# Optimization experiments

Measured on AMD Instinct MI355X. Metric: run time of the kernel, lower is better.

## Reference

```python
import jax, jax.numpy as jnp
import numpy as np

B, S = 32, 256


def _lsa(cost):
    """Rectangular linear sum assignment (Jonker-Volgenant shortest augmenting path),
    equivalent to scipy.optimize.linear_sum_assignment. cost: [R, C] numpy."""
    cost = np.asarray(cost, dtype=np.float64)
    transposed = cost.shape[0] > cost.shape[1]
    if transposed:
        cost = cost.T
    nr, nc = cost.shape  # nr <= nc
    u = np.zeros(nr)
    v = np.zeros(nc)
    path = np.full(nc, -1, dtype=np.int64)
    col4row = np.full(nr, -1, dtype=np.int64)
    row4col = np.full(nc, -1, dtype=np.int64)
    for cur_row in range(nr):
        min_val = 0.0
        i = cur_row
        remaining = np.arange(nc)
        sp = np.full(nc, np.inf)
        SR = np.zeros(nr, dtype=bool)
        SC = np.zeros(nc, dtype=bool)
        sink = -1
        while sink == -1:
            SR[i] = True
            r = min_val + cost[i, remaining] - u[i] - v[remaining]
            better = r < sp[remaining]
            idx_b = remaining[better]
            sp[idx_b] = r[better]
            path[idx_b] = i
            k = int(np.argmin(sp[remaining]))
            j = int(remaining[k])
            min_val = float(sp[j])
            if row4col[j] == -1:
                sink = j
            else:
                i = int(row4col[j])
                SC[j] = True
                remaining = np.delete(remaining, k)
        u[cur_row] += min_val
        others = SR.copy()
        others[cur_row] = False
        rr = np.where(others)[0]
        u[rr] += min_val - sp[col4row[rr]]
        cc = np.where(SC)[0]
        v[cc] += sp[cc] - min_val
        j = sink
        while True:
            i = int(path[j])
            row4col[j] = i
            col4row[i], j = j, int(col4row[i])
            if i == cur_row:
                break
    if transposed:
        rows = col4row
        cols = np.arange(nr)
        order = np.argsort(rows)
        return rows[order], cols[order]
    return np.arange(nr), col4row


def _match(cost_np, valid_np):
    """Per-sample Hungarian matching restricted to valid GT columns.
    Returns padded (pred_idx, gt_idx) [B, maxG] and ngt [B]."""
    Bn = cost_np.shape[0]
    ngt = valid_np.sum(axis=1).astype(np.int64)
    maxG = max(int(ngt.max()), 1)
    pi = np.zeros((Bn, maxG), dtype=np.int64)
    gi = np.zeros((Bn, maxG), dtype=np.int64)
    for b in range(Bn):
        cols = np.where(valid_np[b])[0]
        if len(cols) == 0:
            continue
        r, c = _lsa(cost_np[b][:, cols])
        pi[b, : len(r)] = r
        gi[b, : len(c)] = cols[c]
    return pi, gi, ngt


def _bce_clipped(p, t):
    # matches torch BCELoss: log terms clamped at -100
    return -(t * jnp.clip(jnp.log(p), -100.0) + (1.0 - t) * jnp.clip(jnp.log(1.0 - p), -100.0))


def _loss(pred_strokes, pred_validity, targets, pi, gi, ngt):
    gt_strokes = targets[..., :10]
    gt_val = targets[..., 10:11]
    Bn, maxG = pi.shape
    ngt_f = jnp.asarray(ngt, dtype=pred_strokes.dtype)
    mask = (jnp.arange(maxG)[None, :] < jnp.asarray(ngt)[:, None]).astype(pred_strokes.dtype)  # [B, maxG]
    bidx = np.arange(Bn)[:, None]
    mp = pred_strokes[bidx, pi]  # [B, maxG, 10]
    mg = gt_strokes[bidx, gi]    # [B, maxG, 10]
    # per-sample L1 means over matched pairs (coord: first 8 dims, width: last 2)
    coord = (jnp.abs(mp[..., :8] - mg[..., :8]).sum(-1) * mask).sum(-1) / jnp.maximum(ngt_f * 8.0, 1.0)
    width = (jnp.abs(mp[..., 8:10] - mg[..., 8:10]).sum(-1) * mask).sum(-1) / jnp.maximum(ngt_f * 2.0, 1.0)
    bce = _bce_clipped(pred_validity, gt_val).mean(axis=(1, 2))  # global validity BCE per sample
    # if num_gt == 0 the original only adds the validity BCE
    loss_b = jnp.where(ngt_f > 0, 5.0 * coord + 1.0 * width + 1.0 * bce, bce)
    return loss_b.mean()


def setup_inputs() -> dict:
    key = jax.random.key(0)
    k1, k2, k3, k4 = jax.random.split(key, 4)
    pred_strokes = jax.random.normal(k1, (B, S, 10), dtype=jnp.float32)
    pred_validity = jax.random.uniform(k2, (B, S, 1), dtype=jnp.float32, minval=1e-4, maxval=1.0 - 1e-4)
    gt_strokes = jax.random.normal(k3, (B, S, 10), dtype=jnp.float32)
    gt_valid = (jax.random.uniform(k4, (B, S, 1)) < 0.3).astype(jnp.float32)
    targets = jnp.concatenate([gt_strokes, gt_valid], axis=-1)
    return {"pred_strokes": pred_strokes, "pred_validity": pred_validity, "targets": targets}


def reference(pred_strokes, pred_validity, targets):
    gt_strokes = targets[..., :10]
    gt_val = targets[..., 10:11]
    # vectorized pairwise cost: 5 * L1(coord) + 1 * L1(width), [B, S, S]
    coord_c = jnp.abs(pred_strokes[:, :, None, :8] - gt_strokes[:, None, :, :8]).sum(-1)
    width_c = jnp.abs(pred_strokes[:, :, None, 8:10] - gt_strokes[:, None, :, 8:10]).sum(-1)
    cost = 5.0 * coord_c + width_c
    pi, gi, ngt = _match(np.asarray(cost), np.asarray(gt_val[..., 0]) > 0.5)
    return _loss(pred_strokes, pred_validity, targets, pi, gi, ngt)
```

## Files before the change

### kernel.cpp

```cpp
#include <hip/hip_runtime.h>
#include <math.h>

#define BN 32
#define SN 256
#define CAP 96
#define NT  256

#define KINF 0xFF800000u
#define KMAX 0xFFFFFFFFu

__device__ __forceinline__ unsigned f2k(float f) {
    unsigned b = __float_as_uint(f);
    return (b & 0x80000000u) ? ~b : (b | 0x80000000u);
}
__device__ __forceinline__ float k2f(unsigned k) {
    unsigned b = (k & 0x80000000u) ? (k ^ 0x80000000u) : ~k;
    return __uint_as_float(b);
}
__device__ __forceinline__ int sel4(int a0, int a1, int a2, int a3, int s) {
    int x01 = (s & 1) ? a1 : a0;
    int x23 = (s & 1) ? a3 : a2;
    return (s & 2) ? x23 : x01;
}
#define DPP_MIN(x, ctrl) do {                                                    \
    unsigned _t = (unsigned)__builtin_amdgcn_update_dpp((int)(x), (int)(x),      \
                                                        (ctrl), 0xF, 0xF, false);\
    if (_t < (x)) (x) = _t;                                                      \
} while (0)
#define DPP_MIN2(m1, m2, ctrl) do {                                              \
    unsigned _o1 = (unsigned)__builtin_amdgcn_update_dpp(-1, (int)(m1),          \
                                                         (ctrl), 0xF, 0xF, false);\
    unsigned _o2 = (unsigned)__builtin_amdgcn_update_dpp(-1, (int)(m2),          \
                                                         (ctrl), 0xF, 0xF, false);\
    unsigned _hi = (m1) > _o1 ? (m1) : _o1;                                      \
    (m1) = (m1) < _o1 ? (m1) : _o1;                                              \
    unsigned _s  = (m2) < _o2 ? (m2) : _o2;                                      \
    (m2) = _s < _hi ? _s : _hi;                                                  \
} while (0)
#define DPP_CHAIN_MIN2(a,b) do { DPP_MIN2(a,b,0x111); DPP_MIN2(a,b,0x112); DPP_MIN2(a,b,0x114); \
                                 DPP_MIN2(a,b,0x118); DPP_MIN2(a,b,0x142); DPP_MIN2(a,b,0x143); } while (0)

__device__ __forceinline__ unsigned waveMinU32(unsigned x) {
    DPP_MIN(x, 0x111); DPP_MIN(x, 0x112); DPP_MIN(x, 0x114); DPP_MIN(x, 0x118);
    unsigned a = (unsigned)__builtin_amdgcn_readlane((int)x, 15);
    unsigned b = (unsigned)__builtin_amdgcn_readlane((int)x, 31);
    unsigned c = (unsigned)__builtin_amdgcn_readlane((int)x, 47);
    unsigned d = (unsigned)__builtin_amdgcn_readlane((int)x, 63);
    unsigned ab = a < b ? a : b, cd = c < d ? c : d;
    return ab < cd ? ab : cd;
}

__device__ __forceinline__ float costf(const float* pb, const float* gc) {
    float c = 0.f;
    #pragma unroll
    for (int d = 0; d < 8; ++d) c += fabsf(pb[d] - gc[d]);
    float w = fabsf(pb[8] - gc[8]) + fabsf(pb[9] - gc[9]);
    return 5.0f * c + w;
}
__device__ __forceinline__ void pickLowest(unsigned long long n0, unsigned long long n1,
                                           unsigned long long n2, unsigned long long n3,
                                           int& lm, int& slot) {
    int l0 = n0 ? __builtin_ctzll(n0) : 64;
    int l1 = n1 ? __builtin_ctzll(n1) : 64;
    int l2 = n2 ? __builtin_ctzll(n2) : 64;
    int l3 = n3 ? __builtin_ctzll(n3) : 64;
    int a  = l0 < l1 ? l0 : l1;
    int c  = l2 < l3 ? l2 : l3;
    lm   = a < c ? a : c;
    slot = (l0 == lm) ? 0 : (l1 == lm) ? 1 : (l2 == lm) ? 2 : 3;
}

__global__ __launch_bounds__(NT) void detr_kernel(
    const float* __restrict__ pred_strokes,
    const float* __restrict__ pred_validity,
    const float* __restrict__ targets,
    float* __restrict__ out)
{
    extern __shared__ __align__(16) float sC[];
    __shared__ __align__(16) float sPred[SN * 10];
    __shared__ __align__(16) float sRowC[SN * 10];
    __shared__ float sU[SN];
    __shared__ float sVal[SN];
    __shared__ int   sJ[SN];
    __shared__ int   sFree[SN];
    __shared__ int   sCr4[SN];
    __shared__ float sRed[12];
    __shared__ int   sNgt;

    const int b = blockIdx.x, tid = threadIdx.x, lane = tid & 63, wid = tid >> 6;

    {
        const float4* gp = (const float4*)(pred_strokes + (size_t)b * SN * 10);
        float4* sp4 = (float4*)sPred;
        for (int t = tid; t < SN * 10 / 4; t += NT) sp4[t] = gp[t];
        const float4* gt = (const float4*)(targets + (size_t)b * SN * 11);
        float4* st4 = (float4*)sC;
        for (int t = tid; t < SN * 11 / 4; t += NT) st4[t] = gt[t];
    }
    __syncthreads();

    if (wid == 0) {
        const float* tmpT = sC;
        int ng = 0;
        #pragma unroll
        for (int s = 0; s < 4; ++s) {
            int   pos = s * 64 + lane;
            float tv  = tmpT[pos * 11 + 10];
            sVal[pos] = tv;
            bool  val = tv > 0.5f;
            unsigned long long m = __ballot(val);
            if (val) {
                int r = ng + (int)__popcll(m & ((1ull << lane) - 1ull));
                #pragma unroll
                for (int d = 0; d < 10; ++d) sRowC[r * 10 + d] = tmpT[pos * 11 + d];
            }
            ng += (int)__popcll(m);
        }
        if (lane == 0) sNgt = ng;
    }
    __syncthreads();
    const int ngt = sNgt;

    __align__(16) float prf[40];
    #pragma unroll
    for (int t = 0; t < 10; ++t) ((float4*)prf)[t] = ((const float4*)sPred)[lane * 10 + t];

    float bces;
    {
        float pv  = pred_validity[(size_t)b * SN + tid];
        float tv  = sVal[tid];
        float lp  = logf(pv);       if (lp  < -100.f) lp  = -100.f;
        float l1p = logf(1.f - pv); if (l1p < -100.f) l1p = -100.f;
        bces = -(tv * lp + (1.f - tv) * l1p);
    }

    for (int r = wid; r < ngt; r += 4) {
        const float* gp = &sRowC[r * 10];
        float gc[10];
        #pragma unroll
        for (int d = 0; d < 10; ++d) gc[d] = gp[d];
        float4 cc;
        cc.x = costf(prf +  0, gc);
        cc.y = costf(prf + 10, gc);
        cc.z = costf(prf + 20, gc);
        cc.w = costf(prf + 30, gc);
        if (r < CAP) ((float4*)sC)[r * 64 + lane] = cc;

        unsigned q0 = f2k(cc.x), q1 = f2k(cc.y), q2 = f2k(cc.z), q3 = f2k(cc.w);
        unsigned bk = q0; int bs = 0;
        if (q1 < bk) { bk = q1; bs = 1; }
        if (q2 < bk) { bk = q2; bs = 2; }
        if (q3 < bk) { bk = q3; bs = 3; }
        unsigned minK = waveMinU32(bk);
        unsigned long long mm = __ballot(bk == minK);
        int lm   = __builtin_ctzll(mm);
        int slot = __builtin_amdgcn_readlane(bs, lm);
        if (lane == 0) { sU[r] = k2f(minK); sJ[r] = lm * 4 + slot; }
    }
    __syncthreads();

    if (wid == 0) {
        float v0 = 0.f, v1 = 0.f, v2 = 0.f, v3 = 0.f;
        int   rv0 = -1, rv1 = -1, rv2 = -1, rv3 = -1;
        int   cr0 = -1, cr1 = -1, cr2 = -1, cr3 = -1;
        int   p0 = -1, p1 = -1, p2 = -1, p3 = -1;
        float sc0 = 0.f, sc1 = 0.f, sc2 = 0.f, sc3 = 0.f;
        int   nfree = 0;

        #define ASSIGN_COL(J, R) { int _l=(J)>>2, _s=(J)&3; bool _o=(lane==_l);      \
            switch(_s){ case 0: if(_o) rv0=(R); break; case 1: if(_o) rv1=(R); break;\
                        case 2: if(_o) rv2=(R); break; default: if(_o) rv3=(R); } }
        #define ASSIGN_ROW(R, J) { int _l=(R)>>2, _s=(R)&3; bool _o=(lane==_l);      \
            switch(_s){ case 0: if(_o) cr0=(J); break; case 1: if(_o) cr1=(J); break;\
                        case 2: if(_o) cr2=(J); break; default: if(_o) cr3=(J); } }
        #define READ_RV(LM, SL) __builtin_amdgcn_readlane(sel4(rv0,rv1,rv2,rv3,(SL)), (LM))
        #define LOADROW(I, CW)                                                   \
            if ((I) < CAP) (CW) = ((const float4*)sC)[(I) * 64 + lane];          \
            else {                                                               \
                float gc[10];                                                    \
                _Pragma("unroll")                                                \
                for (int d = 0; d < 10; ++d) gc[d] = sRowC[(I) * 10 + d];        \
                (CW).x = costf(prf +  0, gc); (CW).y = costf(prf + 10, gc);      \
                (CW).z = costf(prf + 20, gc); (CW).w = costf(prf + 30, gc);      \
            }

        int jr[4];
        #pragma unroll
        for (int s = 0; s < 4; ++s) jr[s] = sJ[s * 64 + lane];

        for (int r = 0; r < ngt; ++r) {
            int js = __builtin_amdgcn_readlane(sel4(jr[0], jr[1], jr[2], jr[3], r >> 6), r & 63);
            int lm = js >> 2, slot = js & 3;
            int rn = READ_RV(lm, slot);
            if (rn < 0) {
                ASSIGN_COL(js, r)
                ASSIGN_ROW(r, js)
            } else {
                if (lane == 0) sFree[nfree] = r;
                nfree++;
            }
        }

        int cnt = nfree;
        for (int pass = 0; pass < 2 && cnt > 0; ++pass) {
            int newc = 0;
            for (int idx = 0; idx < cnt; ++idx) {
                const int r = sFree[idx];
                float4 cw;
                LOADROW(r, cw)
                unsigned q0 = f2k(cw.x - v0), q1 = f2k(cw.y - v1);
                unsigned q2 = f2k(cw.z - v2), q3 = f2k(cw.w - v3);
                unsigned a1 = q0 < q1 ? q0 : q1, a2 = q0 < q1 ? q1 : q0;
                unsigned b1 = q2 < q3 ? q2 : q3, b2 = q2 < q3 ? q3 : q2;
                unsigned m1 = a1 < b1 ? a1 : b1;
                unsigned hi = a1 < b1 ? b1 : a1;
                unsigned l2 = a2 < b2 ? a2 : b2;
                unsigned m2 = l2 < hi ? l2 : hi;
                DPP_CHAIN_MIN2(m1, m2);
                unsigned u1k = (unsigned)__builtin_amdgcn_readlane((int)m1, 63);
                unsigned u2k = (unsigned)__builtin_amdgcn_readlane((int)m2, 63);

                unsigned long long n0 = __ballot(q0 == u1k);
                unsigned long long n1 = __ballot(q1 == u1k);
                unsigned long long n2 = __ballot(q2 == u1k);
                unsigned long long n3 = __ballot(q3 == u1k);
                int lm, slot;
                pickLowest(n0, n1, n2, n3, lm, slot);
                int j1 = lm * 4 + slot;
                int i1 = READ_RV(lm, slot);

                if (u1k != u2k) {
                    float du = k2f(u1k) - k2f(u2k);
                    bool own = (lane == (j1 >> 2));
                    switch (j1 & 3) {
                        case 0:  if (own) v0 += du; break;
                        case 1:  if (own) v1 += du; break;
                        case 2:  if (own) v2 += du; break;
                        default: if (own) v3 += du; break;
                    }
                    if (lane == 0) sU[r] = k2f(u2k);
                } else {
                    if (i1 >= 0) {
                        switch (slot) {
                            case 0:  n0 &= ~(1ull << lm); break;
                            case 1:  n1 &= ~(1ull << lm); break;
                            case 2:  n2 &= ~(1ull << lm); break;
                            default: n3 &= ~(1ull << lm); break;
                        }
                        pickLowest(n0, n1, n2, n3, lm, slot);
                        j1 = lm * 4 + slot;
                        i1 = READ_RV(lm, slot);
                    }
                    if (lane == 0) sU[r] = k2f(u1k);
                }

                ASSIGN_COL(j1, r)
                ASSIGN_ROW(r, j1)
                if (i1 >= 0) {
                    if (lane == 0) sFree[newc] = i1;
                    newc++;
                }
            }
            cnt = newc;
        }

        for (int fi = 0; fi < cnt; ++fi) {
            const int cur = sFree[fi];
            unsigned k0 = KINF, k1 = KINF, k2 = KINF, k3 = KINF;
            int   scm  = 0;
            float minv = 0.f;
            int   i    = cur;
            int   sink;

            float4 cw;
            LOADROW(i, cw)
            float ui = sU[i];

            for (;;) {
                #define RELAX(S, CS, KS, PS, VS)                                 \
                {                                                                \
                    float rr = ((minv + CS) - ui) - VS;                          \
                    unsigned kr = f2k(rr);                                       \
                    bool upd = (kr < KS) && !((scm >> S) & 1);                   \
                    if (upd) { KS = kr; PS = i; }                                \
                }
                RELAX(0, cw.x, k0, p0, v0)
                RELAX(1, cw.y, k1, p1, v1)
                RELAX(2, cw.z, k2, p2, v2)
                RELAX(3, cw.w, k3, p3, v3)
                #undef RELAX

                unsigned bk = k0 < k1 ? k0 : k1;
                unsigned bc = k2 < k3 ? k2 : k3;
                if (bc < bk) bk = bc;
                unsigned minK = waveMinU32(bk);

                unsigned long long m0 = __ballot(k0 == minK);
                unsigned long long m1m = __ballot(k1 == minK);
                unsigned long long m2m = __ballot(k2 == minK);
                unsigned long long m3m = __ballot(k3 == minK);
                int lm, slot;
                pickLowest(m0, m1m, m2m, m3m, lm, slot);
                int bj = lm * 4 + slot;

                int rn = READ_RV(lm, slot);
                if (rn < 0) { sink = bj; minv = k2f(minK); break; }
                i = rn;

                float4 cw2;
                LOADROW(i, cw2)
                float ui2 = sU[i];

                minv = k2f(minK);
                bool own = (lane == lm);
                switch (slot) {
                    case 0:  if (own) { scm |= 1; k0 = KMAX; sc0 = minv; } break;
                    case 1:  if (own) { scm |= 2; k1 = KMAX; sc1 = minv; } break;
                    case 2:  if (own) { scm |= 4; k2 = KMAX; sc2 = minv; } break;
                    default: if (own) { scm |= 8; k3 = KMAX; sc3 = minv; } break;
                }
                cw = cw2; ui = ui2;
            }

            if (lane == 0) sU[cur] += minv;
            if (scm & 1) { sU[rv0] += minv - sc0; v0 += sc0 - minv; }
            if (scm & 2) { sU[rv1] += minv - sc1; v1 += sc1 - minv; }
            if (scm & 4) { sU[rv2] += minv - sc2; v2 += sc2 - minv; }
            if (scm & 8) { sU[rv3] += minv - sc3; v3 += sc3 - minv; }

            int j = sink;
            for (;;) {
                int sj = j & 3, lj = j >> 2;
                int i2 = __builtin_amdgcn_readlane(sel4(p0, p1, p2, p3, sj), lj);
                ASSIGN_COL(j, i2)
                int si = i2 & 3, li = i2 >> 2;
                int tmp = __builtin_amdgcn_readlane(sel4(cr0, cr1, cr2, cr3, si), li);
                ASSIGN_ROW(i2, j)
                j = tmp;
                if (i2 == cur) break;
            }
        }

        ((int4*)sCr4)[lane] = make_int4(cr0, cr1, cr2, cr3);
    }
    __syncthreads();

    float coordv = 0.f, widthv = 0.f;
    if (tid < ngt) {
        int p = sCr4[tid];
        const float* pp = &sPred[p * 10];
        const float* gg = &sRowC[tid * 10];
        float c = 0.f;
        #pragma unroll
        for (int d = 0; d < 8; ++d) c += fabsf(pp[d] - gg[d]);
        coordv = c;
        widthv = fabsf(pp[8] - gg[8]) + fabsf(pp[9] - gg[9]);
    }
    #pragma unroll
    for (int m = 1; m <= 32; m <<= 1) {
        coordv += __shfl_xor(coordv, m, 64);
        widthv += __shfl_xor(widthv, m, 64);
        bces   += __shfl_xor(bces,   m, 64);
    }
    if (lane == 0) {
        sRed[wid * 3 + 0] = coordv;
        sRed[wid * 3 + 1] = widthv;
        sRed[wid * 3 + 2] = bces;
    }
    __syncthreads();
    if (tid == 0) {
        float C = 0.f, W = 0.f, Bc = 0.f;
        #pragma unroll
        for (int w = 0; w < 4; ++w) {
            C += sRed[w * 3 + 0]; W += sRed[w * 3 + 1]; Bc += sRed[w * 3 + 2];
        }
        float bcem = Bc / (float)SN;
        float lb = (ngt > 0)
                 ? (5.f * C / (8.f * (float)ngt) + W / (2.f * (float)ngt) + bcem)
                 : bcem;
        atomicAdd(out, lb * (1.0f / (float)BN));
    }
}

extern "C" void kernel_launch(void* const* d_in, const int* in_sizes, int n_in,
                              void* d_out, int out_size, void* d_ws, size_t ws_size,
                              hipStream_t stream) {
    const float* pred_strokes  = (const float*)d_in[0];
    const float* pred_validity = (const float*)d_in[1];
    const float* targets       = (const float*)d_in[2];
    float* out = (float*)d_out;

    const int dynBytes = CAP * SN * 4;
    (void)hipFuncSetAttribute((const void*)detr_kernel,
                              hipFuncAttributeMaxDynamicSharedMemorySize, dynBytes);
    detr_kernel<<<BN, NT, dynBytes, stream>>>(pred_strokes, pred_validity, targets, out);
}
```

Measured before the change: 123.4 us.

## Use packed value-index wave argmin and parallel atomic column claiming in init

Replaces the separate wave min reduction and four-ballot argmin with a single DPP reduction over (key, column) pairs, which returns the minimum and its lowest column index together inside the Dijkstra loop. The serial column-reduction pass that assigned each row's best column one by one is replaced by per-wave atomicMin claims into shared memory, followed by a ballot-compacted free-row list built in parallel. This shortens the serial critical path of the single-wave assignment. The pair reduction costs two DPP moves per step plus 64-bit compares, and the claiming order (lowest row wins) differs from the previous sequential first-come rule.

New measurement: 115.0 us. 1.07x faster.

```diff
diff --git a/kernel.cpp b/kernel.cpp
--- a/kernel.cpp
+++ b/kernel.cpp
@@ -8,6 +8,7 @@
 
 #define KINF 0xFF800000u
 #define KMAX 0xFFFFFFFFu
+#define CLNONE 0x7FFFFFFF
 
 __device__ __forceinline__ unsigned f2k(float f) {
     unsigned b = __float_as_uint(f);
@@ -40,14 +41,31 @@
 #define DPP_CHAIN_MIN2(a,b) do { DPP_MIN2(a,b,0x111); DPP_MIN2(a,b,0x112); DPP_MIN2(a,b,0x114); \
                                  DPP_MIN2(a,b,0x118); DPP_MIN2(a,b,0x142); DPP_MIN2(a,b,0x143); } while (0)
 
-__device__ __forceinline__ unsigned waveMinU32(unsigned x) {
-    DPP_MIN(x, 0x111); DPP_MIN(x, 0x112); DPP_MIN(x, 0x114); DPP_MIN(x, 0x118);
-    unsigned a = (unsigned)__builtin_amdgcn_readlane((int)x, 15);
-    unsigned b = (unsigned)__builtin_amdgcn_readlane((int)x, 31);
-    unsigned c = (unsigned)__builtin_amdgcn_readlane((int)x, 47);
-    unsigned d = (unsigned)__builtin_amdgcn_readlane((int)x, 63);
-    unsigned ab = a < b ? a : b, cd = c < d ? c : d;
-    return ab < cd ? ab : cd;
+#define DPP_MINPAIR(HI, LO, ctrl) do {                                           \
+    unsigned _oh = (unsigned)__builtin_amdgcn_update_dpp(-1, (int)(HI),          \
+                                                         (ctrl), 0xF, 0xF, false);\
+    unsigned _ol = (unsigned)__builtin_amdgcn_update_dpp(-1, (int)(LO),          \
+                                                         (ctrl), 0xF, 0xF, false);\
+    bool _lt = (_oh < (HI)) || ((_oh == (HI)) && (_ol < (LO)));                  \
+    if (_lt) { (HI) = _oh; (LO) = _ol; }                                         \
+} while (0)
+
+__device__ __forceinline__ unsigned long long waveMinPair(unsigned hi, unsigned lo) {
+    DPP_MINPAIR(hi, lo, 0x111);
+    DPP_MINPAIR(hi, lo, 0x112);
+    DPP_MINPAIR(hi, lo, 0x114);
+    DPP_MINPAIR(hi, lo, 0x118);
+    unsigned long long p0 = ((unsigned long long)(unsigned)__builtin_amdgcn_readlane((int)hi, 15) << 32)
+                          |  (unsigned)__builtin_amdgcn_readlane((int)lo, 15);
+    unsigned long long p1 = ((unsigned long long)(unsigned)__builtin_amdgcn_readlane((int)hi, 31) << 32)
+                          |  (unsigned)__builtin_amdgcn_readlane((int)lo, 31);
+    unsigned long long p2 = ((unsigned long long)(unsigned)__builtin_amdgcn_readlane((int)hi, 47) << 32)
+                          |  (unsigned)__builtin_amdgcn_readlane((int)lo, 47);
+    unsigned long long p3 = ((unsigned long long)(unsigned)__builtin_amdgcn_readlane((int)hi, 63) << 32)
+                          |  (unsigned)__builtin_amdgcn_readlane((int)lo, 63);
+    unsigned long long a = p0 < p1 ? p0 : p1;
+    unsigned long long c = p2 < p3 ? p2 : p3;
+    return a < c ? a : c;
 }
 
 __device__ __forceinline__ float costf(const float* pb, const float* gc) {
@@ -82,6 +100,7 @@
     __shared__ float sU[SN];
     __shared__ float sVal[SN];
     __shared__ int   sJ[SN];
+    __shared__ int   sClaim[SN];
     __shared__ int   sFree[SN];
     __shared__ int   sCr4[SN];
     __shared__ float sRed[12];
@@ -96,6 +115,8 @@
         const float4* gt = (const float4*)(targets + (size_t)b * SN * 11);
         float4* st4 = (float4*)sC;
         for (int t = tid; t < SN * 11 / 4; t += NT) st4[t] = gt[t];
+        sClaim[tid] = CLNONE;
+        sJ[tid]     = 0;
     }
     __syncthreads();
 
@@ -134,6 +155,8 @@
         bces = -(tv * lp + (1.f - tv) * l1p);
     }
 
+    const unsigned c0i = (unsigned)(lane * 4), c1i = c0i + 1, c2i = c0i + 2, c3i = c0i + 3;
+
     for (int r = wid; r < ngt; r += 4) {
         const float* gp = &sRowC[r * 10];
         float gc[10];
@@ -147,25 +170,47 @@
         if (r < CAP) ((float4*)sC)[r * 64 + lane] = cc;
 
         unsigned q0 = f2k(cc.x), q1 = f2k(cc.y), q2 = f2k(cc.z), q3 = f2k(cc.w);
-        unsigned bk = q0; int bs = 0;
-        if (q1 < bk) { bk = q1; bs = 1; }
-        if (q2 < bk) { bk = q2; bs = 2; }
-        if (q3 < bk) { bk = q3; bs = 3; }
-        unsigned minK = waveMinU32(bk);
-        unsigned long long mm = __ballot(bk == minK);
-        int lm   = __builtin_ctzll(mm);
-        int slot = __builtin_amdgcn_readlane(bs, lm);
-        if (lane == 0) { sU[r] = k2f(minK); sJ[r] = lm * 4 + slot; }
+        unsigned bhi = q0, bcol = c0i;
+        if (q1 < bhi) { bhi = q1; bcol = c1i; }
+        if (q2 < bhi) { bhi = q2; bcol = c2i; }
+        if (q3 < bhi) { bhi = q3; bcol = c3i; }
+        unsigned long long mk = waveMinPair(bhi, bcol);
+        int      mj = (int)(unsigned)mk;
+        if (lane == 0) {
+            sU[r] = k2f((unsigned)(mk >> 32));
+            sJ[r] = mj;
+            atomicMin(&sClaim[mj], r);
+        }
     }
     __syncthreads();
 
     if (wid == 0) {
         float v0 = 0.f, v1 = 0.f, v2 = 0.f, v3 = 0.f;
-        int   rv0 = -1, rv1 = -1, rv2 = -1, rv3 = -1;
-        int   cr0 = -1, cr1 = -1, cr2 = -1, cr3 = -1;
+        float sc0 = 0.f, sc1 = 0.f, sc2 = 0.f, sc3 = 0.f;
         int   p0 = -1, p1 = -1, p2 = -1, p3 = -1;
-        float sc0 = 0.f, sc1 = 0.f, sc2 = 0.f, sc3 = 0.f;
-        int   nfree = 0;
+
+        int4 cl = ((const int4*)sClaim)[lane];
+        int rv0 = (cl.x != CLNONE) ? cl.x : -1;
+        int rv1 = (cl.y != CLNONE) ? cl.y : -1;
+        int rv2 = (cl.z != CLNONE) ? cl.z : -1;
+        int rv3 = (cl.w != CLNONE) ? cl.w : -1;
+        int4 j4 = ((const int4*)sJ)[lane];
+        int cr0 = (lane * 4 + 0 < ngt && sClaim[j4.x] == lane * 4 + 0) ? j4.x : -1;
+        int cr1 = (lane * 4 + 1 < ngt && sClaim[j4.y] == lane * 4 + 1) ? j4.y : -1;
+        int cr2 = (lane * 4 + 2 < ngt && sClaim[j4.z] == lane * 4 + 2) ? j4.z : -1;
+        int cr3 = (lane * 4 + 3 < ngt && sClaim[j4.w] == lane * 4 + 3) ? j4.w : -1;
+
+        int nfree = 0;
+        #pragma unroll
+        for (int s = 0; s < 4; ++s) {
+            int  pos = s * 64 + lane;
+            int  cs  = (s == 0) ? cr0 : (s == 1) ? cr1 : (s == 2) ? cr2 : cr3;
+            bool fr = (pos < ngt) && (sClaim[sJ[pos]] != pos);
+            (void)cs;
+            unsigned long long m = __ballot(fr);
+            if (fr) sFree[nfree + (int)__popcll(m & ((1ull << lane) - 1ull))] = pos;
+            nfree += (int)__popcll(m);
+        }
 
         #define ASSIGN_COL(J, R) { int _l=(J)>>2, _s=(J)&3; bool _o=(lane==_l);      \
             switch(_s){ case 0: if(_o) rv0=(R); break; case 1: if(_o) rv1=(R); break;\
@@ -183,23 +228,6 @@
                 (CW).x = costf(prf +  0, gc); (CW).y = costf(prf + 10, gc);      \
                 (CW).z = costf(prf + 20, gc); (CW).w = costf(prf + 30, gc);      \
             }
-
-        int jr[4];
-        #pragma unroll
-        for (int s = 0; s < 4; ++s) jr[s] = sJ[s * 64 + lane];
-
-        for (int r = 0; r < ngt; ++r) {
-            int js = __builtin_amdgcn_readlane(sel4(jr[0], jr[1], jr[2], jr[3], r >> 6), r & 63);
-            int lm = js >> 2, slot = js & 3;
-            int rn = READ_RV(lm, slot);
-            if (rn < 0) {
-                ASSIGN_COL(js, r)
-                ASSIGN_ROW(r, js)
-            } else {
-                if (lane == 0) sFree[nfree] = r;
-                nfree++;
-            }
-        }
 
         int cnt = nfree;
         for (int pass = 0; pass < 2 && cnt > 0; ++pass) {
@@ -290,28 +318,23 @@
                 RELAX(3, cw.w, k3, p3, v3)
                 #undef RELAX
 
-                unsigned bk = k0 < k1 ? k0 : k1;
-                unsigned bc = k2 < k3 ? k2 : k3;
-                if (bc < bk) bk = bc;
-                unsigned minK = waveMinU32(bk);
-
-                unsigned long long m0 = __ballot(k0 == minK);
-                unsigned long long m1m = __ballot(k1 == minK);
-                unsigned long long m2m = __ballot(k2 == minK);
-                unsigned long long m3m = __ballot(k3 == minK);
-                int lm, slot;
-                pickLowest(m0, m1m, m2m, m3m, lm, slot);
-                int bj = lm * 4 + slot;
+                unsigned bhi = k0, bcol = c0i;
+                if (k1 < bhi) { bhi = k1; bcol = c1i; }
+                if (k2 < bhi) { bhi = k2; bcol = c2i; }
+                if (k3 < bhi) { bhi = k3; bcol = c3i; }
+                unsigned long long mk = waveMinPair(bhi, bcol);
+                int bj = (int)(unsigned)mk;
+                int lm = bj >> 2, slot = bj & 3;
 
                 int rn = READ_RV(lm, slot);
-                if (rn < 0) { sink = bj; minv = k2f(minK); break; }
+                if (rn < 0) { sink = bj; minv = k2f((unsigned)(mk >> 32)); break; }
                 i = rn;
 
                 float4 cw2;
                 LOADROW(i, cw2)
                 float ui2 = sU[i];
 
-                minv = k2f(minK);
+                minv = k2f((unsigned)(mk >> 32));
                 bool own = (lane == lm);
                 switch (slot) {
                     case 0:  if (own) { scm |= 1; k0 = KMAX; sc0 = minv; } break;
```
